# Performance work log

Measured on AMD Instinct MI355X. Metric: run time of the kernel, lower is better.

## Reference

```python
import jax, jax.numpy as jnp
import numpy as np

EPS = 1e-8

def setup_inputs() -> dict:
    key = jax.random.key(0)
    k1, k2, k3, k4 = jax.random.split(key, 4)
    b, in_c, out_c, style_c, k, h, w = 8, 512, 512, 512, 3, 64, 64
    return {
        "input": jax.random.normal(k1, (b, in_c, h, w), dtype=jnp.float32),
        "style": jax.random.normal(k2, (b, style_c), dtype=jnp.float32),
        "w_affine": jax.random.normal(k3, (in_c, style_c), dtype=jnp.float32),  # Linear weight, init N(0,1), runtime-scaled
        "b_affine": jnp.ones((1, in_c), dtype=jnp.float32),                     # Bias init_value=1.0
        "w_conv": jax.random.normal(k4, (out_c, in_c, k, k), dtype=jnp.float32),
    }

def reference(input, style, w_affine, b_affine, w_conv):
    b, in_c, h, w = input.shape
    out_c, _, kh, kw = w_conv.shape
    # Equalized-LR runtime scales (lr_mul=1):
    affine_scale = 1.0 / (w_affine.shape[1] ** 0.5)          # he_std for Linear
    conv_scale = 1.0 / ((in_c * kh * kw) ** 0.5)             # he_std for conv weight
    # affine: Linear + Bias (bias initialized to 1.0)
    s = style @ w_affine.T * affine_scale + b_affine          # [b, in_c]
    # modulate: per-sample weight tensor [b, out_c, in_c, kh, kw]
    wgt = s[:, None, :, None, None] * (w_conv * conv_scale)[None]
    # demodulate
    demod = jax.lax.rsqrt(jnp.sum(wgt * wgt, axis=(2, 3, 4), keepdims=True) + EPS)
    wgt = wgt * demod
    # grouped conv with groups = batch (stride=1, padding=1)
    x = input.reshape(1, b * in_c, h, w)
    wgt = wgt.reshape(b * out_c, in_c, kh, kw)
    out = jax.lax.conv_general_dilated(
        x, wgt,
        window_strides=(1, 1),
        padding=[(1, 1), (1, 1)],
        dimension_numbers=("NCHW", "OIHW", "NCHW"),
        feature_group_count=b,
    )
    return out.reshape(b, out_c, h, w)
```

## Files before the change

### kernel.cpp

```cpp
#include <hip/hip_runtime.h>
#include <hip/hip_bf16.h>

#define BB 8
#define CIN 512
#define COUT 512
#define HH 64
#define WW 64

#define AFF_SCALE 0.044194173824159216f
#define CONV_SCALE 0.014731391274719736f
#define CONV_SCALE2 (1.0f/4608.0f)

typedef short s16x8 __attribute__((ext_vector_type(8)));
typedef float f32x4 __attribute__((ext_vector_type(4)));

__device__ __forceinline__ unsigned short f2bf(float f) {
  __hip_bfloat16 h = __float2bfloat16(f);
  return *reinterpret_cast<unsigned short*>(&h);
}

__global__ __launch_bounds__(256) void affine_kernel(
    const float* __restrict__ style, const float* __restrict__ wa,
    const float* __restrict__ ba, float* __restrict__ smod) {
  int wid  = (blockIdx.x << 2) + (threadIdx.x >> 6);
  int lane = threadIdx.x & 63;
  int b  = wid >> 9;
  int ic = wid & 511;
  const float* s = style + b * CIN;
  const float* w = wa + (size_t)ic * CIN;
  float sum = 0.f;
#pragma unroll
  for (int k = 0; k < CIN / 64; ++k) sum += s[lane + 64 * k] * w[lane + 64 * k];
#pragma unroll
  for (int off = 32; off; off >>= 1) sum += __shfl_down(sum, off, 64);
  if (lane == 0) smod[wid] = sum * AFF_SCALE + ba[ic];
}

__global__ __launch_bounds__(256) void wsq_kernel(
    const float* __restrict__ wc, float* __restrict__ wsq) {
  int i = blockIdx.x * 256 + threadIdx.x;
  const float* p = wc + (size_t)i * 9;
  float s = 0.f;
#pragma unroll
  for (int k = 0; k < 9; ++k) { float v = p[k]; s += v * v; }
  wsq[i] = s;
}

__global__ __launch_bounds__(256) void demod_kernel(
    const float* __restrict__ smod, const float* __restrict__ wsq,
    float* __restrict__ demod) {
  int wid  = (blockIdx.x << 2) + (threadIdx.x >> 6);
  int lane = threadIdx.x & 63;
  int b  = wid >> 9;
  int oc = wid & 511;
  const float* s = smod + b * CIN;
  const float* w = wsq + (size_t)oc * CIN;
  float sum = 0.f;
#pragma unroll
  for (int k = 0; k < CIN / 64; ++k) {
    float sv = s[lane + 64 * k];
    sum += sv * sv * w[lane + 64 * k];
  }
#pragma unroll
  for (int off = 32; off; off >>= 1) sum += __shfl_down(sum, off, 64);
  if (lane == 0) demod[wid] = rsqrtf(sum * CONV_SCALE2 + 1e-8f) * CONV_SCALE;
}

__global__ __launch_bounds__(256) void premod_kernel(
    const float* __restrict__ xin, const float* __restrict__ smod,
    ushort* __restrict__ xt) {
  int n = blockIdx.x * 256 + threadIdx.x;
  int kg = n & 3;
  int x  = (n >> 2) & 63;
  int y  = (n >> 8) & 63;
  int g  = (n >> 14) & 15;
  int b  = n >> 18;
  int ic0 = g * 32 + kg * 8;
  const float* sp = smod + b * CIN + ic0;
  const float* xp = xin + (((size_t)b * CIN + ic0) * HH + y) * WW + x;
  s16x8 o;
#pragma unroll
  for (int j = 0; j < 8; ++j) {
    float v = xp[(size_t)j * HH * WW] * sp[j];
    o[j] = (short)f2bf(v);
  }
  *(s16x8*)(xt + (size_t)n * 8) = o;
}

__global__ __launch_bounds__(256) void wpack_kernel(
    const float* __restrict__ wc, ushort* __restrict__ wfrag) {
  int n = blockIdx.x * 256 + threadIdx.x;
  int l = n & 63;
  int rem = n >> 6;
  int ocg = rem & 31;
  int rem2 = rem >> 5;
  int tap = rem2 % 9;
  int g   = rem2 / 9;
  int oc  = ocg * 16 + (l & 15);
  int ic0 = g * 32 + (l >> 4) * 8;
  int kh = tap / 3, kw = tap - kh * 3;
  s16x8 o;
#pragma unroll
  for (int j = 0; j < 8; ++j) {
    float v = wc[((size_t)oc * CIN + ic0 + j) * 9 + kh * 3 + kw];
    o[j] = (short)f2bf(v);
  }
  *(s16x8*)(wfrag + (size_t)n * 8) = o;
}

#define XS_ROWSZ 4608
#define XS_SIZE  (6 * XS_ROWSZ)
#define WS_SIZE  8192

__global__ __launch_bounds__(256, 2) void conv_mfma(
    const ushort* __restrict__ xt,
    const ushort* __restrict__ wfrag,
    const float* __restrict__ demod,
    float* __restrict__ out) {
  __shared__ char lds[2 * XS_SIZE + 2 * WS_SIZE];
  char* wsb = lds + 2 * XS_SIZE;

  int tid = threadIdx.x;
  int l = tid & 63, w = tid >> 6;
  int bid = blockIdx.x;
  int ocb = bid & 3;
  int b   = (bid >> 2) & 7;
  int yt  = bid >> 5;
  int y0  = yt * 4;

  f32x4 acc[8][4];
#pragma unroll
  for (int i = 0; i < 8; ++i)
#pragma unroll
    for (int j = 0; j < 4; ++j) acc[i][j] = f32x4{0.f, 0.f, 0.f, 0.f};

  if (tid < 96) {
    int r    = tid >> 4;
    int kg   = (tid >> 2) & 3;
    int side = (tid >> 1) & 1;
    int buf  = tid & 1;
    int ct   = side ? 65 : 0;
    int off  = buf * XS_SIZE + r * XS_ROWSZ + (ct >> 3) * 512 + kg * 128 + (ct & 7) * 16;
    *(int4*)(lds + off) = int4{0, 0, 0, 0};
  }

  int sx = tid & 63;
  int skg = w;
  int sct = sx + 1;
  int xs_woff = (sct >> 3) * 512 + skg * 128 + (sct & 7) * 16;

  {
    const int4* wsrc = (const int4*)(wfrag + (size_t)(ocb * 8) * 512);
    int4 wv0 = wsrc[tid];
    int4 wv1 = wsrc[tid + 256];
#pragma unroll
    for (int r = 0; r < 6; ++r) {
      int gy = y0 - 1 + r;
      int4 t = {0, 0, 0, 0};
      if (gy >= 0 && gy < HH)
        t = *(const int4*)(xt + ((((size_t)(b * 16 + 0) * 4096) + gy * 64 + sx) * 32 + skg * 8));
      *(int4*)(lds + r * XS_ROWSZ + xs_woff) = t;
    }
    *(int4*)(wsb + tid * 16) = wv0;
    *(int4*)(wsb + tid * 16 + 4096) = wv1;
  }
  __syncthreads();

  int4 xv[6];
  for (int g = 0; g < 16; ++g) {
    char* xs_r = lds + (g & 1) * XS_SIZE;
    char* xs_w = lds + ((g & 1) ^ 1) * XS_SIZE;
#pragma unroll
    for (int tap = 0; tap < 9; ++tap) {
      const int k = g * 9 + tap;
      char* ws_cur = wsb + (k & 1) * WS_SIZE;
      char* ws_nxt = wsb + ((k & 1) ^ 1) * WS_SIZE;

      if (tap == 0 && g < 15) {
#pragma unroll
        for (int r = 0; r < 6; ++r) {
          int gy = y0 - 1 + r;
          xv[r] = int4{0, 0, 0, 0};
          if (gy >= 0 && gy < HH)
            xv[r] = *(const int4*)(xt + ((((size_t)(b * 16 + g + 1) * 4096) + gy * 64 + sx) * 32 + skg * 8));
        }
      }
      int4 nv0, nv1;
      if (k < 143) {
        const int4* wsrc = (const int4*)(wfrag + ((size_t)(k + 1) * 32 + ocb * 8) * 512);
        nv0 = wsrc[tid];
        nv1 = wsrc[tid + 256];
      }

      const int dy = tap / 3 - 1, dx = tap % 3 - 1;
      const int rb = w + 1 + dy;
      s16x8 bfr[4];
#pragma unroll
      for (int fn = 0; fn < 4; ++fn) {
        int c2 = fn * 16 + (l & 15) + dx + 1;
        bfr[fn] = *(const s16x8*)(xs_r + rb * XS_ROWSZ + (c2 >> 3) * 512 + (l >> 4) * 128 + (c2 & 7) * 16);
      }

      __builtin_amdgcn_s_setprio(1);
#pragma unroll
      for (int fm = 0; fm < 8; ++fm) {
        s16x8 afr = *(const s16x8*)(ws_cur + fm * 1024 + l * 16);
#pragma unroll
        for (int fn = 0; fn < 4; ++fn)
          acc[fm][fn] = __builtin_amdgcn_mfma_f32_16x16x32_bf16(afr, bfr[fn], acc[fm][fn], 0, 0, 0);
      }
      __builtin_amdgcn_s_setprio(0);

      if (k < 143) {
        *(int4*)(ws_nxt + tid * 16) = nv0;
        *(int4*)(ws_nxt + tid * 16 + 4096) = nv1;
      }
      if (tap == 8 && g < 15) {
#pragma unroll
        for (int r = 0; r < 6; ++r)
          *(int4*)(xs_w + r * XS_ROWSZ + xs_woff) = xv[r];
      }

      asm volatile("s_waitcnt lgkmcnt(0)" ::: "memory");
      __builtin_amdgcn_sched_barrier(0);
      __builtin_amdgcn_s_barrier();
      __builtin_amdgcn_sched_barrier(0);
    }
  }

  int oc_base = ocb * 128;
  int gy = y0 + w;
#pragma unroll
  for (int fm = 0; fm < 8; ++fm) {
#pragma unroll
    for (int r = 0; r < 4; ++r) {
      int oc = oc_base + fm * 16 + (l >> 4) * 4 + r;
      float dm = demod[b * COUT + oc];
#pragma unroll
      for (int fn = 0; fn < 4; ++fn) {
        out[(((size_t)b * COUT + oc) * 4096) + gy * 64 + fn * 16 + (l & 15)] =
            acc[fm][fn][r] * dm;
      }
    }
  }
}

extern "C" void kernel_launch(void* const* d_in, const int* in_sizes, int n_in,
                              void* d_out, int out_size, void* d_ws, size_t ws_size,
                              hipStream_t stream) {
  const float* input = (const float*)d_in[0];
  const float* style = (const float*)d_in[1];
  const float* wa    = (const float*)d_in[2];
  const float* ba    = (const float*)d_in[3];
  const float* wconv = (const float*)d_in[4];
  float* out = (float*)d_out;

  float* smod  = (float*)d_ws;
  float* demod = smod + BB * CIN;
  float* wsq   = demod + BB * COUT;
  ushort* wfrag = (ushort*)(wsq + (size_t)COUT * CIN);
  ushort* xt    = wfrag + (size_t)16 * 9 * 32 * 64 * 8;

  affine_kernel<<<BB * CIN / 4, 256, 0, stream>>>(style, wa, ba, smod);
  wsq_kernel<<<COUT * CIN / 256, 256, 0, stream>>>(wconv, wsq);
  demod_kernel<<<BB * COUT / 4, 256, 0, stream>>>(smod, wsq, demod);
  wpack_kernel<<<16 * 9 * 32 * 64 / 256, 256, 0, stream>>>(wconv, wfrag);
  premod_kernel<<<BB * 16 * 64 * 64 * 4 / 256, 256, 0, stream>>>(input, smod, xt);
  conv_mfma<<<BB * 4 * 16, 256, 0, stream>>>(xt, wfrag, demod, out);
}
```

Before: 156.6 us.

## Load conv weight fragments straight into registers, drop per-tap LDS staging and barriers

Weight fragments for each tap are now loaded from global memory directly into a double-buffered register array per wave, instead of being staged through shared memory. This removes the shared-memory weight buffers and the barrier after every tap; only one barrier per input-channel group remains, after the next input tile is written to shared memory. The prefetch of the next input tile moves to tap 7. In exchange, each of the four waves fetches the same weight data from L2 separately, and register pressure rises by 64 VGPRs for the weight buffers. The final prefetch reads slightly past the packed weight buffer into the following workspace region, and those values are never used.

New measurement: 184.4 us. +17.8%, slower.

```diff
diff --git a/kernel.cpp b/kernel.cpp
--- a/kernel.cpp
+++ b/kernel.cpp
@@ -110,15 +110,13 @@
 
 #define XS_ROWSZ 4608
 #define XS_SIZE  (6 * XS_ROWSZ)
-#define WS_SIZE  8192
 
 __global__ __launch_bounds__(256, 2) void conv_mfma(
     const ushort* __restrict__ xt,
     const ushort* __restrict__ wfrag,
     const float* __restrict__ demod,
     float* __restrict__ out) {
-  __shared__ char lds[2 * XS_SIZE + 2 * WS_SIZE];
-  char* wsb = lds + 2 * XS_SIZE;
+  __shared__ char lds[2 * XS_SIZE];
 
   int tid = threadIdx.x;
   int l = tid & 63, w = tid >> 6;
@@ -149,82 +147,81 @@
   int sct = sx + 1;
   int xs_woff = (sct >> 3) * 512 + skg * 128 + (sct & 7) * 16;
 
-  {
-    const int4* wsrc = (const int4*)(wfrag + (size_t)(ocb * 8) * 512);
-    int4 wv0 = wsrc[tid];
-    int4 wv1 = wsrc[tid + 256];
-#pragma unroll
-    for (int r = 0; r < 6; ++r) {
-      int gy = y0 - 1 + r;
-      int4 t = {0, 0, 0, 0};
-      if (gy >= 0 && gy < HH)
-        t = *(const int4*)(xt + ((((size_t)(b * 16 + 0) * 4096) + gy * 64 + sx) * 32 + skg * 8));
-      *(int4*)(lds + r * XS_ROWSZ + xs_woff) = t;
-    }
-    *(int4*)(wsb + tid * 16) = wv0;
-    *(int4*)(wsb + tid * 16 + 4096) = wv1;
+  const ushort* wlane = wfrag + (size_t)(ocb * 8) * 512 + (size_t)l * 8;
+
+  s16x8 wA[2][8];
+#pragma unroll
+  for (int fm = 0; fm < 8; ++fm)
+    wA[0][fm] = *(const s16x8*)(wlane + fm * 512);
+
+#pragma unroll
+  for (int r = 0; r < 6; ++r) {
+    int gy = y0 - 1 + r;
+    int4 t = {0, 0, 0, 0};
+    if (gy >= 0 && gy < HH)
+      t = *(const int4*)(xt + ((((size_t)(b * 16 + 0) * 4096) + gy * 64 + sx) * 32 + skg * 8));
+    *(int4*)(lds + r * XS_ROWSZ + xs_woff) = t;
   }
   __syncthreads();
 
   int4 xv[6];
-  for (int g = 0; g < 16; ++g) {
-    char* xs_r = lds + (g & 1) * XS_SIZE;
-    char* xs_w = lds + ((g & 1) ^ 1) * XS_SIZE;
-#pragma unroll
-    for (int tap = 0; tap < 9; ++tap) {
-      const int k = g * 9 + tap;
-      char* ws_cur = wsb + (k & 1) * WS_SIZE;
-      char* ws_nxt = wsb + ((k & 1) ^ 1) * WS_SIZE;
-
-      if (tap == 0 && g < 15) {
-#pragma unroll
-        for (int r = 0; r < 6; ++r) {
-          int gy = y0 - 1 + r;
-          xv[r] = int4{0, 0, 0, 0};
-          if (gy >= 0 && gy < HH)
-            xv[r] = *(const int4*)(xt + ((((size_t)(b * 16 + g + 1) * 4096) + gy * 64 + sx) * 32 + skg * 8));
+  for (int g2 = 0; g2 < 8; ++g2) {
+#pragma unroll
+    for (int gg = 0; gg < 2; ++gg) {
+      const int g = g2 * 2 + gg;
+      char* xs_r = lds + gg * XS_SIZE;
+      char* xs_w = lds + (gg ^ 1) * XS_SIZE;
+#pragma unroll
+      for (int tap = 0; tap < 9; ++tap) {
+        const int kpar = (gg * 9 + tap) & 1;
+
+        {
+          const ushort* wp = wlane + (size_t)(g * 9 + tap + 1) * 16384;
+#pragma unroll
+          for (int fm = 0; fm < 8; ++fm)
+            wA[kpar ^ 1][fm] = *(const s16x8*)(wp + fm * 512);
+        }
+
+        if (tap == 7) {
+          int gn = (g < 15) ? g + 1 : 15;
+#pragma unroll
+          for (int r = 0; r < 6; ++r) {
+            int gy = y0 - 1 + r;
+            int4 t = {0, 0, 0, 0};
+            if (gy >= 0 && gy < HH)
+              t = *(const int4*)(xt + ((((size_t)(b * 16 + gn) * 4096) + gy * 64 + sx) * 32 + skg * 8));
+            xv[r] = t;
+          }
+        }
+
+        const int dy = tap / 3 - 1, dx = tap % 3 - 1;
+        const int rb = w + 1 + dy;
+        s16x8 bfr[4];
+#pragma unroll
+        for (int fn = 0; fn < 4; ++fn) {
+          int c2 = fn * 16 + (l & 15) + dx + 1;
+          bfr[fn] = *(const s16x8*)(xs_r + rb * XS_ROWSZ + (c2 >> 3) * 512 + (l >> 4) * 128 + (c2 & 7) * 16);
+        }
+
+        __builtin_amdgcn_s_setprio(1);
+#pragma unroll
+        for (int fm = 0; fm < 8; ++fm) {
+#pragma unroll
+          for (int fn = 0; fn < 4; ++fn)
+            acc[fm][fn] = __builtin_amdgcn_mfma_f32_16x16x32_bf16(wA[kpar][fm], bfr[fn], acc[fm][fn], 0, 0, 0);
+        }
+        __builtin_amdgcn_s_setprio(0);
+
+        if (tap == 8) {
+#pragma unroll
+          for (int r = 0; r < 6; ++r)
+            *(int4*)(xs_w + r * XS_ROWSZ + xs_woff) = xv[r];
+          asm volatile("s_waitcnt lgkmcnt(0)" ::: "memory");
+          __builtin_amdgcn_sched_barrier(0);
+          __builtin_amdgcn_s_barrier();
+          __builtin_amdgcn_sched_barrier(0);
         }
       }
-      int4 nv0, nv1;
-      if (k < 143) {
-        const int4* wsrc = (const int4*)(wfrag + ((size_t)(k + 1) * 32 + ocb * 8) * 512);
-        nv0 = wsrc[tid];
-        nv1 = wsrc[tid + 256];
-      }
-
-      const int dy = tap / 3 - 1, dx = tap % 3 - 1;
-      const int rb = w + 1 + dy;
-      s16x8 bfr[4];
-#pragma unroll
-      for (int fn = 0; fn < 4; ++fn) {
-        int c2 = fn * 16 + (l & 15) + dx + 1;
-        bfr[fn] = *(const s16x8*)(xs_r + rb * XS_ROWSZ + (c2 >> 3) * 512 + (l >> 4) * 128 + (c2 & 7) * 16);
-      }
-
-      __builtin_amdgcn_s_setprio(1);
-#pragma unroll
-      for (int fm = 0; fm < 8; ++fm) {
-        s16x8 afr = *(const s16x8*)(ws_cur + fm * 1024 + l * 16);
-#pragma unroll
-        for (int fn = 0; fn < 4; ++fn)
-          acc[fm][fn] = __builtin_amdgcn_mfma_f32_16x16x32_bf16(afr, bfr[fn], acc[fm][fn], 0, 0, 0);
-      }
-      __builtin_amdgcn_s_setprio(0);
-
-      if (k < 143) {
-        *(int4*)(ws_nxt + tid * 16) = nv0;
-        *(int4*)(ws_nxt + tid * 16 + 4096) = nv1;
-      }
-      if (tap == 8 && g < 15) {
-#pragma unroll
-        for (int r = 0; r < 6; ++r)
-          *(int4*)(xs_w + r * XS_ROWSZ + xs_woff) = xv[r];
-      }
-
-      asm volatile("s_waitcnt lgkmcnt(0)" ::: "memory");
-      __builtin_amdgcn_sched_barrier(0);
-      __builtin_amdgcn_s_barrier();
-      __builtin_amdgcn_sched_barrier(0);
     }
   }
 
```
